# Optimization experiments

Measured on AMD Instinct MI355X. Metric: run time of the kernel, lower is better.

## Reference

```python
import jax, jax.numpy as jnp
import numpy as np

N = 30000          # num nodes
E = 480000         # num edges (before self-loops)
D_MODEL = 128
HEADS = 8
HEAD_DIM = D_MODEL // HEADS  # 16
LAYERS = 7
NUM_LABELS = 2
NEG_SLOPE = 0.2


def setup_inputs() -> dict:
    key = jax.random.key(0)
    ks = jax.random.split(key, 10)
    s = 0.05
    x = jax.random.normal(ks[0], (N, D_MODEL), dtype=jnp.float32)
    edge_index = jax.random.randint(ks[1], (2, E), 0, N, dtype=jnp.int64)
    Wl = jax.random.normal(ks[2], (LAYERS, D_MODEL, D_MODEL), dtype=jnp.float32) * s
    bl = jnp.zeros((LAYERS, D_MODEL), dtype=jnp.float32)
    Wr = jax.random.normal(ks[3], (LAYERS, D_MODEL, D_MODEL), dtype=jnp.float32) * s
    br = jnp.zeros((LAYERS, D_MODEL), dtype=jnp.float32)
    att = jax.random.normal(ks[4], (LAYERS, HEADS, HEAD_DIM), dtype=jnp.float32) * s
    bias = jnp.zeros((LAYERS, D_MODEL), dtype=jnp.float32)
    W_out = jax.random.normal(ks[5], (D_MODEL, 1), dtype=jnp.float32) * s
    b_out = jnp.zeros((1,), dtype=jnp.float32)
    return {"x": x, "edge_index": edge_index, "Wl": Wl, "bl": bl,
            "Wr": Wr, "br": br, "att": att, "bias": bias,
            "W_out": W_out, "b_out": b_out}


def _gatv2_layer(x, Wl, bl, Wr, br, att, bias, src, dst):
    # x: [N, d]; src/dst: [E'] (with self-loops). GATv2 (dropout off / eval).
    xl = (x @ Wl + bl).reshape(N, HEADS, HEAD_DIM)  # source transform
    xr = (x @ Wr + br).reshape(N, HEADS, HEAD_DIM)  # target transform
    m = xl[src] + xr[dst]                           # [E', H, D]
    e = jnp.einsum('ehd,hd->eh', jax.nn.leaky_relu(m, NEG_SLOPE), att)  # [E', H]
    # segment softmax over destination nodes (self-loops => no empty segments)
    emax = jax.ops.segment_max(e, dst, num_segments=N)  # [N, H]
    ee = jnp.exp(e - emax[dst])
    denom = jax.ops.segment_sum(ee, dst, num_segments=N)  # [N, H]
    alpha = ee / (denom[dst] + 1e-16)                      # [E', H]
    out = jax.ops.segment_sum(alpha[:, :, None] * xl[src], dst, num_segments=N)
    return out.reshape(N, D_MODEL) + bias


def reference(x, edge_index, Wl, bl, Wr, br, att, bias, W_out, b_out):
    loops = jnp.arange(N, dtype=edge_index.dtype)
    src = jnp.concatenate([edge_index[0], loops])  # add_self_loops=True (PyG default)
    dst = jnp.concatenate([edge_index[1], loops])
    for i in range(LAYERS):
        x = _gatv2_layer(x, Wl[i], bl[i], Wr[i], br[i], att[i], bias[i], src, dst)
    y = x @ W_out + b_out            # [N, 1]
    return y[:NUM_LABELS, 0].reshape(1, -1)  # [1, num_labels]
```

## Files before the change

kernel.cpp:

```cpp
#include <hip/hip_runtime.h>
#include <hip/hip_fp16.h>

#define NN 30000
#define ER 480000
#define ET 510000
#define D 128
#define NH 8
#define HD 16
#define NL 7
#define SLOPE 0.2f
#define NB_SCAN 118

typedef unsigned int uint32;
typedef unsigned short ushort;
typedef __attribute__((ext_vector_type(8))) short short8;
typedef __attribute__((ext_vector_type(4))) float f32x4;
typedef _Float16 h2_t __attribute__((ext_vector_type(2)));

#if defined(__has_builtin)
#if __has_builtin(__builtin_amdgcn_fdot2)
#define HAS_FDOT2 1
#endif
#endif

__device__ inline ushort f2bf(float f) {
    uint32 u = __float_as_uint(f);
    return (ushort)((u + 0x7fffu + ((u >> 16) & 1u)) >> 16);
}
__device__ inline float bf2f(ushort h) {
    return __uint_as_float(((uint32)h) << 16);
}

__device__ inline __half2 hmax2p(__half2 a, __half2 b) {
    h2_t x = *reinterpret_cast<h2_t*>(&a), y = *reinterpret_cast<h2_t*>(&b);
    h2_t r;
    r[0] = x[0] > y[0] ? x[0] : y[0];
    r[1] = x[1] > y[1] ? x[1] : y[1];
    return *reinterpret_cast<__half2*>(&r);
}
__device__ inline __half2 hmin2p(__half2 a, __half2 b) {
    h2_t x = *reinterpret_cast<h2_t*>(&a), y = *reinterpret_cast<h2_t*>(&b);
    h2_t r;
    r[0] = x[0] < y[0] ? x[0] : y[0];
    r[1] = x[1] < y[1] ? x[1] : y[1];
    return *reinterpret_cast<__half2*>(&r);
}


__global__ void k_zero(int* __restrict__ p, int n) {
    int i = blockIdx.x * 256 + threadIdx.x;
    if (i < n) p[i] = 0;
}

__global__ void k_hist(const int* __restrict__ ei, int* __restrict__ counts) {
    int i = blockIdx.x * 256 + threadIdx.x;
    if (i >= ET) return;
    int dst = (i < ER) ? ei[ER + i] : (i - ER);
    atomicAdd(&counts[dst], 1);
}

__global__ __launch_bounds__(256) void k_scan1(const int* __restrict__ counts,
                                               int* __restrict__ offsets,
                                               int* __restrict__ partials) {
    int t = threadIdx.x;
    int i = blockIdx.x * 256 + t;
    int v = (i < NN) ? counts[i] : 0;
    int lane = t & 63;
    int incl = v;
#pragma unroll
    for (int d = 1; d < 64; d <<= 1) {
        int u = __shfl_up(incl, d);
        if (lane >= d) incl += u;
    }
    __shared__ int ws[4];
    if (lane == 63) ws[t >> 6] = incl;
    __syncthreads();
    int wid = t >> 6;
    int base = 0;
    if (wid > 0) base += ws[0];
    if (wid > 1) base += ws[1];
    if (wid > 2) base += ws[2];
    if (i < NN) offsets[i] = base + incl - v;
    if (t == 255) partials[blockIdx.x] = base + incl;
}

__global__ __launch_bounds__(128) void k_scan2(int* __restrict__ partials,
                                               int* __restrict__ offsets) {
    int t = threadIdx.x;
    int v = (t < NB_SCAN) ? partials[t] : 0;
    int lane = t & 63;
    int incl = v;
#pragma unroll
    for (int d = 1; d < 64; d <<= 1) {
        int u = __shfl_up(incl, d);
        if (lane >= d) incl += u;
    }
    __shared__ int w0;
    if (t == 63) w0 = incl;
    __syncthreads();
    int base = (t >= 64) ? w0 : 0;
    if (t < NB_SCAN) partials[t] = base + incl - v;
    if (t == 127) offsets[NN] = base + incl;
}

__global__ void k_scan3(const int* __restrict__ partials, int* __restrict__ offsets,
                        int* __restrict__ cursor) {
    int i = blockIdx.x * 256 + threadIdx.x;
    if (i < NN) {
        int o = offsets[i] + partials[blockIdx.x];
        offsets[i] = o;
        cursor[i] = o;
    }
}

__global__ void k_scatter(const int* __restrict__ ei, int* __restrict__ cursor,
                          int* __restrict__ srcs) {
    int i = blockIdx.x * 256 + threadIdx.x;
    if (i >= ET) return;
    int src, dst;
    if (i < ER) { src = ei[i]; dst = ei[ER + i]; }
    else        { src = i - ER; dst = src; }
    int pos = atomicAdd(&cursor[dst], 1);
    srcs[pos] = src;
}


__global__ __launch_bounds__(256) void k_wprep(const float* __restrict__ Wl,
                                               const float* __restrict__ Wr,
                                               ushort* __restrict__ Wth,
                                               ushort* __restrict__ Wtl) {
    int bx = blockIdx.x;
    int layer = bx >> 3;
    int n0 = (bx & 7) * 32;
    const float* WL = Wl + (size_t)layer * D * D;
    const float* WR = Wr + (size_t)layer * D * D;
    ushort* th = Wth + (size_t)layer * 256 * 128;
    ushort* tl = Wtl + (size_t)layer * 256 * 128;
    for (int idx = threadIdx.x; idx < 32 * 128; idx += 256) {
        int n = n0 + (idx >> 7);
        int k = idx & 127;
        float w = (n < 128) ? WL[k * 128 + n] : WR[k * 128 + (n - 128)];
        ushort h = f2bf(w);
        ushort e = f2bf(w - bf2f(h));
        th[n * 128 + k] = h;
        tl[n * 128 + k] = e;
    }
}


__global__ void k_xsplit(const float* __restrict__ x,
                         ushort* __restrict__ xh, ushort* __restrict__ xe) {
    int i = (blockIdx.x * 256 + threadIdx.x) * 4;
    if (i >= NN * D) return;
    float4 f = *reinterpret_cast<const float4*>(x + i);
    ushort4 h, e;
    h.x = f2bf(f.x); e.x = f2bf(f.x - bf2f(h.x));
    h.y = f2bf(f.y); e.y = f2bf(f.y - bf2f(h.y));
    h.z = f2bf(f.z); e.z = f2bf(f.z - bf2f(h.z));
    h.w = f2bf(f.w); e.w = f2bf(f.w - bf2f(h.w));
    *reinterpret_cast<ushort4*>(xh + i) = h;
    *reinterpret_cast<ushort4*>(xe + i) = e;
}


__global__ __launch_bounds__(256) void k_mm(const ushort* __restrict__ Xh,
                                            const ushort* __restrict__ Xe,
                                            const ushort* __restrict__ Wth,
                                            const ushort* __restrict__ Wtl,
                                            const float* __restrict__ bl,
                                            const float* __restrict__ br,
                                            ushort* __restrict__ xlh,
                                            ushort* __restrict__ xrh) {
    __shared__ ushort Wh[64][136];
    __shared__ ushort We[64][136];
    const int row0 = blockIdx.x * 64;
    const int nq = blockIdx.y;
    const int tid = threadIdx.x;
    const int wv = tid >> 6;
    const int l  = tid & 63;
    const int lr = l & 15;
    const int kg = (l >> 4) * 8;

    {
        int nn = tid >> 2;
        int ch = tid & 3;
        const ushort* wh = Wth + (size_t)(nq * 64 + nn) * 128;
        const ushort* wl = Wtl + (size_t)(nq * 64 + nn) * 128;
#pragma unroll
        for (int pass = 0; pass < 4; ++pass) {
            int ko = (ch * 4 + pass) * 8;
            *reinterpret_cast<uint4*>(&Wh[nn][ko]) = *reinterpret_cast<const uint4*>(wh + ko);
            *reinterpret_cast<uint4*>(&We[nn][ko]) = *reinterpret_cast<const uint4*>(wl + ko);
        }
    }
    short8 Ah[4], Ae[4];
    {
        int row = row0 + wv * 16 + lr; if (row >= NN) row = NN - 1;
        const ushort* xh = Xh + (size_t)row * D;
        const ushort* xe = Xe + (size_t)row * D;
#pragma unroll
        for (int kc = 0; kc < 4; ++kc) {
            Ah[kc] = *reinterpret_cast<const short8*>(xh + kc * 32 + kg);
            Ae[kc] = *reinterpret_cast<const short8*>(xe + kc * 32 + kg);
        }
    }
    __syncthreads();

    f32x4 acc[4] = {};
#pragma unroll
    for (int kc = 0; kc < 4; ++kc) {
#pragma unroll
        for (int nc = 0; nc < 4; ++nc) {
            short8 Bh = *reinterpret_cast<const short8*>(&Wh[nc * 16 + lr][kc * 32 + kg]);
            short8 Be = *reinterpret_cast<const short8*>(&We[nc * 16 + lr][kc * 32 + kg]);
            acc[nc] = __builtin_amdgcn_mfma_f32_16x16x32_bf16(Ah[kc], Bh, acc[nc], 0, 0, 0);
            acc[nc] = __builtin_amdgcn_mfma_f32_16x16x32_bf16(Ah[kc], Be, acc[nc], 0, 0, 0);
            acc[nc] = __builtin_amdgcn_mfma_f32_16x16x32_bf16(Ae[kc], Bh, acc[nc], 0, 0, 0);
        }
    }
    const int rbase = row0 + wv * 16 + (l >> 4) * 4;
#pragma unroll
    for (int nc = 0; nc < 4; ++nc) {
        int g = nq * 64 + nc * 16 + lr;
        float bb = (g < 128) ? bl[g] : br[g - 128];
        ushort* dst = (g < 128) ? (xlh + g) : (xrh + (g - 128));
#pragma unroll
        for (int j = 0; j < 4; ++j) {
            int row = rbase + j;
            if (row < NN)
                dst[(size_t)row * D] = __half_as_ushort(__float2half_rn(acc[nc][j] + bb));
        }
    }
}


__device__ inline float score_dot(__half2 lr2, __half2 a2) {
#ifdef HAS_FDOT2
    h2_t x = *reinterpret_cast<h2_t*>(&lr2);
    h2_t a = *reinterpret_cast<h2_t*>(&a2);
    return __builtin_amdgcn_fdot2(x, a, 0.0f, false);
#else
    float2 lf = __half22float2(lr2);
    float2 af = __half22float2(a2);
    return fmaf(lf.x, af.x, lf.y * af.y);
#endif
}

#define FUSED_UPD(vv, sS, aS0, aS1)                                             \
    {                                                                           \
        __half2 vh = *reinterpret_cast<const __half2*>(&(vv));                  \
        __half2 th = __hadd2(vh, rh);                                           \
        __half2 lr2 = __hfma2(hmin2p(th, zero2), slope2, hmax2p(th, zero2));    \
        float e = score_dot(lr2, ah2);                                          \
        e += __shfl_xor(e, 1);                                                  \
        e += __shfl_xor(e, 2);                                                  \
        e += __shfl_xor(e, 4);                                                  \
        float p = __expf(e);                                                    \
        float2 vf = __half22float2(vh);                                         \
        sS += p;                                                                \
        aS0 = fmaf(p, vf.x, aS0);                                               \
        aS1 = fmaf(p, vf.y, aS1);                                               \
    }

__global__ __launch_bounds__(256) void k_fused(const int* __restrict__ offsets,
                                               const int* __restrict__ srcs,
                                               const uint32* __restrict__ xlh,
                                               const uint32* __restrict__ xrh,
                                               const float* __restrict__ att,
                                               const float* __restrict__ bias,
                                               uint32* __restrict__ outH,
                                               uint32* __restrict__ outE) {
    const int lane = threadIdx.x & 63;
    const int n = blockIdx.x * 4 + (threadIdx.x >> 6);
    const int off = offsets[n];
    const int deg = offsets[n + 1] - off;

    uint32 ru = xrh[(size_t)n * 64 + lane];
    const __half2 rh = *reinterpret_cast<const __half2*>(&ru);
    float2 aa = *reinterpret_cast<const float2*>(&att[2 * lane]);
    const __half2 ah2 = __floats2half2_rn(aa.x, aa.y);
    const __half2 zero2 = __float2half2_rn(0.f);
    const __half2 slope2 = __float2half2_rn(SLOPE);

    float sA = 0.f, accA0 = 0.f, accA1 = 0.f;
    float sB = 0.f, accB0 = 0.f, accB1 = 0.f;

    int i = 0;
    int peel = (4 - (off & 3)) & 3;
    if (peel > deg) peel = deg;
    for (; i < peel; ++i) {
        uint32 vv = xlh[(size_t)srcs[off + i] * 64 + lane];
        FUSED_UPD(vv, sA, accA0, accA1);
    }
    for (; i + 8 <= deg; i += 8) {
        int4 sq0 = *reinterpret_cast<const int4*>(&srcs[off + i]);
        int4 sq1 = *reinterpret_cast<const int4*>(&srcs[off + i + 4]);
        int sa[8] = {sq0.x, sq0.y, sq0.z, sq0.w, sq1.x, sq1.y, sq1.z, sq1.w};
        uint32 vv[8];
#pragma unroll
        for (int j = 0; j < 8; ++j) vv[j] = xlh[(size_t)sa[j] * 64 + lane];
        FUSED_UPD(vv[0], sA, accA0, accA1);
        FUSED_UPD(vv[1], sB, accB0, accB1);
        FUSED_UPD(vv[2], sA, accA0, accA1);
        FUSED_UPD(vv[3], sB, accB0, accB1);
        FUSED_UPD(vv[4], sA, accA0, accA1);
        FUSED_UPD(vv[5], sB, accB0, accB1);
        FUSED_UPD(vv[6], sA, accA0, accA1);
        FUSED_UPD(vv[7], sB, accB0, accB1);
    }
    for (; i + 4 <= deg; i += 4) {
        int4 sq = *reinterpret_cast<const int4*>(&srcs[off + i]);
        int sa[4] = {sq.x, sq.y, sq.z, sq.w};
        uint32 vv[4];
#pragma unroll
        for (int j = 0; j < 4; ++j) vv[j] = xlh[(size_t)sa[j] * 64 + lane];
        FUSED_UPD(vv[0], sA, accA0, accA1);
        FUSED_UPD(vv[1], sB, accB0, accB1);
        FUSED_UPD(vv[2], sA, accA0, accA1);
        FUSED_UPD(vv[3], sB, accB0, accB1);
    }
    for (; i < deg; ++i) {
        uint32 vv = xlh[(size_t)srcs[off + i] * 64 + lane];
        FUSED_UPD(vv, sA, accA0, accA1);
    }

    float s = sA + sB;
    float inv = 1.f / (s + 1e-16f);
    float2 bb = *reinterpret_cast<const float2*>(&bias[2 * lane]);
    float o0 = (accA0 + accB0) * inv + bb.x;
    float o1 = (accA1 + accB1) * inv + bb.y;
    ushort h0 = f2bf(o0), h1 = f2bf(o1);
    ushort e0 = f2bf(o0 - bf2f(h0)), e1 = f2bf(o1 - bf2f(h1));
    outH[(size_t)n * 64 + lane] = (uint32)h0 | ((uint32)h1 << 16);
    outE[(size_t)n * 64 + lane] = (uint32)e0 | ((uint32)e1 << 16);
}


__global__ void k_out(const ushort* __restrict__ xh, const ushort* __restrict__ xe,
                      const float* __restrict__ Wout, const float* __restrict__ bout,
                      float* __restrict__ y) {
    int lane = threadIdx.x;
#pragma unroll
    for (int i = 0; i < 2; ++i) {
        float x0 = bf2f(xh[i * D + lane]) + bf2f(xe[i * D + lane]);
        float x1 = bf2f(xh[i * D + 64 + lane]) + bf2f(xe[i * D + 64 + lane]);
        float v = x0 * Wout[lane] + x1 * Wout[64 + lane];
        v += __shfl_xor(v, 1); v += __shfl_xor(v, 2); v += __shfl_xor(v, 4);
        v += __shfl_xor(v, 8); v += __shfl_xor(v, 16); v += __shfl_xor(v, 32);
        if (lane == 0) y[i] = v + bout[0];
    }
}


extern "C" void kernel_launch(void* const* d_in, const int* in_sizes, int n_in,
                              void* d_out, int out_size, void* d_ws, size_t ws_size,
                              hipStream_t stream) {
    const float* x_in = (const float*)d_in[0];
    const int*   ei   = (const int*)d_in[1];
    const float* Wl   = (const float*)d_in[2];
    const float* bl   = (const float*)d_in[3];
    const float* Wr   = (const float*)d_in[4];
    const float* br   = (const float*)d_in[5];
    const float* att  = (const float*)d_in[6];
    const float* bias = (const float*)d_in[7];
    const float* Wout = (const float*)d_in[8];
    const float* bout = (const float*)d_in[9];
    float* y = (float*)d_out;

    char* ws = (char*)d_ws;
    size_t o = 0;
    auto alloc = [&](size_t bytes) -> void* {
        void* p = ws + o;
        o = (o + bytes + 255) & ~(size_t)255;
        return p;
    };
    ushort* XhA = (ushort*)alloc((size_t)NN * D * 2);
    ushort* XeA = (ushort*)alloc((size_t)NN * D * 2);
    ushort* XhB = (ushort*)alloc((size_t)NN * D * 2);
    ushort* XeB = (ushort*)alloc((size_t)NN * D * 2);
    ushort* xlh = (ushort*)alloc((size_t)NN * D * 2);
    ushort* xrh = (ushort*)alloc((size_t)NN * D * 2);
    ushort* Wth = (ushort*)alloc((size_t)NL * 256 * 128 * 2);
    ushort* Wtl = (ushort*)alloc((size_t)NL * 256 * 128 * 2);
    int* counts   = (int*)alloc((size_t)NN * 4);
    int* offsets  = (int*)alloc(((size_t)NN + 1) * 4);
    int* cursor   = (int*)alloc((size_t)NN * 4);
    int* srcs     = (int*)alloc((size_t)ET * 4);
    int* partials = (int*)alloc(256 * 4);
    (void)ws_size; (void)in_sizes; (void)n_in; (void)out_size;

    k_zero<<<NB_SCAN, 256, 0, stream>>>(counts, NN);
    k_hist<<<(ET + 255) / 256, 256, 0, stream>>>(ei, counts);
    k_scan1<<<NB_SCAN, 256, 0, stream>>>(counts, offsets, partials);
    k_scan2<<<1, 128, 0, stream>>>(partials, offsets);
    k_scan3<<<NB_SCAN, 256, 0, stream>>>(partials, offsets, cursor);
    k_scatter<<<(ET + 255) / 256, 256, 0, stream>>>(ei, cursor, srcs);
    k_wprep<<<NL * 8, 256, 0, stream>>>(Wl, Wr, Wth, Wtl);
    k_xsplit<<<NN * D / 1024, 256, 0, stream>>>(x_in, XhA, XeA);

    const int mgrid = (NN + 63) / 64;
    for (int i = 0; i < NL; ++i) {
        const ushort* inH = (i & 1) ? XhB : XhA;
        const ushort* inE = (i & 1) ? XeB : XeA;
        ushort* oH = (i & 1) ? XhA : XhB;
        ushort* oE = (i & 1) ? XeA : XeB;
        k_mm<<<dim3(mgrid, 4), 256, 0, stream>>>(inH, inE,
                                                 Wth + (size_t)i * 256 * 128,
                                                 Wtl + (size_t)i * 256 * 128,
                                                 bl + i * D, br + i * D, xlh, xrh);
        k_fused<<<NN / 4, 256, 0, stream>>>(offsets, srcs, (const uint32*)xlh,
                                            (const uint32*)xrh,
                                            att + i * NH * HD, bias + i * D,
                                            (uint32*)oH, (uint32*)oE);
    }
    k_out<<<1, 64, 0, stream>>>(XhB, XeB, Wout, bout, y);
}
```

Before: 427.4 us.

## Split each node's wavefront into two halves processing alternate edges

The fused attention-aggregation kernel now assigns 32 lanes per edge, each handling four features through 8-byte loads, so one wavefront processes two edges at a time (even and odd indices). The two halves are combined with a cross-half shuffle at the end, and only the first half writes the output. The head reduction needs one fewer shuffle step, and the vectorized srcs loads with the alignment peel are replaced by scalar index loads. This is meant to raise memory-level parallelism on the gather and cut per-edge shuffle and exp work, at the cost of half the lanes idling during the epilogue.

```diff
diff --git a/kernel.cpp b/kernel.cpp
--- a/kernel.cpp
+++ b/kernel.cpp
@@ -44,6 +44,18 @@
     r[0] = x[0] < y[0] ? x[0] : y[0];
     r[1] = x[1] < y[1] ? x[1] : y[1];
     return *reinterpret_cast<__half2*>(&r);
+}
+
+__device__ inline float score_dot(__half2 l2, __half2 a2, float acc) {
+#ifdef HAS_FDOT2
+    h2_t x = *reinterpret_cast<h2_t*>(&l2);
+    h2_t a = *reinterpret_cast<h2_t*>(&a2);
+    return __builtin_amdgcn_fdot2(x, a, acc, false);
+#else
+    float2 lf = __half22float2(l2);
+    float2 af = __half22float2(a2);
+    return fmaf(lf.x, af.x, fmaf(lf.y, af.y, acc));
+#endif
 }
 
 
@@ -234,32 +246,25 @@
 }
 
 
-__device__ inline float score_dot(__half2 lr2, __half2 a2) {
-#ifdef HAS_FDOT2
-    h2_t x = *reinterpret_cast<h2_t*>(&lr2);
-    h2_t a = *reinterpret_cast<h2_t*>(&a2);
-    return __builtin_amdgcn_fdot2(x, a, 0.0f, false);
-#else
-    float2 lf = __half22float2(lr2);
-    float2 af = __half22float2(a2);
-    return fmaf(lf.x, af.x, lf.y * af.y);
-#endif
-}
-
-#define FUSED_UPD(vv, sS, aS0, aS1)                                             \
+#define PROC(v)                                                                 \
     {                                                                           \
-        __half2 vh = *reinterpret_cast<const __half2*>(&(vv));                  \
-        __half2 th = __hadd2(vh, rh);                                           \
-        __half2 lr2 = __hfma2(hmin2p(th, zero2), slope2, hmax2p(th, zero2));    \
-        float e = score_dot(lr2, ah2);                                          \
+        __half2 vh0 = *reinterpret_cast<const __half2*>(&(v).x);                \
+        __half2 vh1 = *reinterpret_cast<const __half2*>(&(v).y);                \
+        __half2 t0 = __hadd2(vh0, rh0);                                         \
+        __half2 t1 = __hadd2(vh1, rh1);                                         \
+        __half2 l0 = __hfma2(hmin2p(t0, zero2), slope2, hmax2p(t0, zero2));     \
+        __half2 l1 = __hfma2(hmin2p(t1, zero2), slope2, hmax2p(t1, zero2));     \
+        float e = score_dot(l0, a0, score_dot(l1, a1, 0.f));                    \
         e += __shfl_xor(e, 1);                                                  \
         e += __shfl_xor(e, 2);                                                  \
-        e += __shfl_xor(e, 4);                                                  \
         float p = __expf(e);                                                    \
-        float2 vf = __half22float2(vh);                                         \
-        sS += p;                                                                \
-        aS0 = fmaf(p, vf.x, aS0);                                               \
-        aS1 = fmaf(p, vf.y, aS1);                                               \
+        float2 f0 = __half22float2(vh0);                                        \
+        float2 f1 = __half22float2(vh1);                                        \
+        s += p;                                                                 \
+        acc0 = fmaf(p, f0.x, acc0);                                             \
+        acc1 = fmaf(p, f0.y, acc1);                                             \
+        acc2 = fmaf(p, f1.x, acc2);                                             \
+        acc3 = fmaf(p, f1.y, acc3);                                             \
     }
 
 __global__ __launch_bounds__(256) void k_fused(const int* __restrict__ offsets,
@@ -270,69 +275,67 @@
                                                const float* __restrict__ bias,
                                                uint32* __restrict__ outH,
                                                uint32* __restrict__ outE) {
-    const int lane = threadIdx.x & 63;
-    const int n = blockIdx.x * 4 + (threadIdx.x >> 6);
+    const int tid = threadIdx.x;
+    const int lane = tid & 63;
+    const int half = lane >> 5;
+    const int sl = lane & 31;
+    const int n = blockIdx.x * 4 + (tid >> 6);
     const int off = offsets[n];
     const int deg = offsets[n + 1] - off;
 
-    uint32 ru = xrh[(size_t)n * 64 + lane];
-    const __half2 rh = *reinterpret_cast<const __half2*>(&ru);
-    float2 aa = *reinterpret_cast<const float2*>(&att[2 * lane]);
-    const __half2 ah2 = __floats2half2_rn(aa.x, aa.y);
+    uint2 ru = *reinterpret_cast<const uint2*>(&xrh[(size_t)n * 64 + 2 * sl]);
+    const __half2 rh0 = *reinterpret_cast<const __half2*>(&ru.x);
+    const __half2 rh1 = *reinterpret_cast<const __half2*>(&ru.y);
+    float4 af = *reinterpret_cast<const float4*>(&att[4 * sl]);
+    const __half2 a0 = __floats2half2_rn(af.x, af.y);
+    const __half2 a1 = __floats2half2_rn(af.z, af.w);
     const __half2 zero2 = __float2half2_rn(0.f);
     const __half2 slope2 = __float2half2_rn(SLOPE);
 
-    float sA = 0.f, accA0 = 0.f, accA1 = 0.f;
-    float sB = 0.f, accB0 = 0.f, accB1 = 0.f;
-
-    int i = 0;
-    int peel = (4 - (off & 3)) & 3;
-    if (peel > deg) peel = deg;
-    for (; i < peel; ++i) {
-        uint32 vv = xlh[(size_t)srcs[off + i] * 64 + lane];
-        FUSED_UPD(vv, sA, accA0, accA1);
-    }
-    for (; i + 8 <= deg; i += 8) {
-        int4 sq0 = *reinterpret_cast<const int4*>(&srcs[off + i]);
-        int4 sq1 = *reinterpret_cast<const int4*>(&srcs[off + i + 4]);
-        int sa[8] = {sq0.x, sq0.y, sq0.z, sq0.w, sq1.x, sq1.y, sq1.z, sq1.w};
-        uint32 vv[8];
-#pragma unroll
-        for (int j = 0; j < 8; ++j) vv[j] = xlh[(size_t)sa[j] * 64 + lane];
-        FUSED_UPD(vv[0], sA, accA0, accA1);
-        FUSED_UPD(vv[1], sB, accB0, accB1);
-        FUSED_UPD(vv[2], sA, accA0, accA1);
-        FUSED_UPD(vv[3], sB, accB0, accB1);
-        FUSED_UPD(vv[4], sA, accA0, accA1);
-        FUSED_UPD(vv[5], sB, accB0, accB1);
-        FUSED_UPD(vv[6], sA, accA0, accA1);
-        FUSED_UPD(vv[7], sB, accB0, accB1);
-    }
-    for (; i + 4 <= deg; i += 4) {
-        int4 sq = *reinterpret_cast<const int4*>(&srcs[off + i]);
-        int sa[4] = {sq.x, sq.y, sq.z, sq.w};
-        uint32 vv[4];
-#pragma unroll
-        for (int j = 0; j < 4; ++j) vv[j] = xlh[(size_t)sa[j] * 64 + lane];
-        FUSED_UPD(vv[0], sA, accA0, accA1);
-        FUSED_UPD(vv[1], sB, accB0, accB1);
-        FUSED_UPD(vv[2], sA, accA0, accA1);
-        FUSED_UPD(vv[3], sB, accB0, accB1);
-    }
-    for (; i < deg; ++i) {
-        uint32 vv = xlh[(size_t)srcs[off + i] * 64 + lane];
-        FUSED_UPD(vv, sA, accA0, accA1);
-    }
-
-    float s = sA + sB;
-    float inv = 1.f / (s + 1e-16f);
-    float2 bb = *reinterpret_cast<const float2*>(&bias[2 * lane]);
-    float o0 = (accA0 + accB0) * inv + bb.x;
-    float o1 = (accA1 + accB1) * inv + bb.y;
-    ushort h0 = f2bf(o0), h1 = f2bf(o1);
-    ushort e0 = f2bf(o0 - bf2f(h0)), e1 = f2bf(o1 - bf2f(h1));
-    outH[(size_t)n * 64 + lane] = (uint32)h0 | ((uint32)h1 << 16);
-    outE[(size_t)n * 64 + lane] = (uint32)e0 | ((uint32)e1 << 16);
+    float s = 0.f, acc0 = 0.f, acc1 = 0.f, acc2 = 0.f, acc3 = 0.f;
+
+    int i = half;
+    for (; i + 6 < deg; i += 8) {
+        int s0 = srcs[off + i];
+        int s1 = srcs[off + i + 2];
+        int s2 = srcs[off + i + 4];
+        int s3 = srcs[off + i + 6];
+        uint2 v0 = *reinterpret_cast<const uint2*>(&xlh[(size_t)s0 * 64 + 2 * sl]);
+        uint2 v1 = *reinterpret_cast<const uint2*>(&xlh[(size_t)s1 * 64 + 2 * sl]);
+        uint2 v2 = *reinterpret_cast<const uint2*>(&xlh[(size_t)s2 * 64 + 2 * sl]);
+        uint2 v3 = *reinterpret_cast<const uint2*>(&xlh[(size_t)s3 * 64 + 2 * sl]);
+        PROC(v0); PROC(v1); PROC(v2); PROC(v3);
+    }
+    for (; i < deg; i += 2) {
+        int sid = srcs[off + i];
+        uint2 v = *reinterpret_cast<const uint2*>(&xlh[(size_t)sid * 64 + 2 * sl]);
+        PROC(v);
+    }
+
+    s += __shfl_xor(s, 32);
+    acc0 += __shfl_xor(acc0, 32);
+    acc1 += __shfl_xor(acc1, 32);
+    acc2 += __shfl_xor(acc2, 32);
+    acc3 += __shfl_xor(acc3, 32);
+
+    if (half == 0) {
+        float inv = 1.f / (s + 1e-16f);
+        float4 bb = *reinterpret_cast<const float4*>(&bias[4 * sl]);
+        float o0 = acc0 * inv + bb.x;
+        float o1 = acc1 * inv + bb.y;
+        float o2 = acc2 * inv + bb.z;
+        float o3 = acc3 * inv + bb.w;
+        ushort h0 = f2bf(o0), h1 = f2bf(o1), h2 = f2bf(o2), h3 = f2bf(o3);
+        ushort e0 = f2bf(o0 - bf2f(h0)), e1 = f2bf(o1 - bf2f(h1));
+        ushort e2 = f2bf(o2 - bf2f(h2)), e3 = f2bf(o3 - bf2f(h3));
+        uint2 wh, we;
+        wh.x = (uint32)h0 | ((uint32)h1 << 16);
+        wh.y = (uint32)h2 | ((uint32)h3 << 16);
+        we.x = (uint32)e0 | ((uint32)e1 << 16);
+        we.y = (uint32)e2 | ((uint32)e3 << 16);
+        *reinterpret_cast<uint2*>(&outH[(size_t)n * 64 + 2 * sl]) = wh;
+        *reinterpret_cast<uint2*>(&outE[(size_t)n * 64 + 2 * sl]) = we;
+    }
 }
 
 
```

After: 392.5 us. 8.1% less time.
